# Optimization experiments

Hardware: AMD Instinct MI355X
Metric: run time of the kernel (lower is better)

## Reference

```python
import jax, jax.numpy as jnp
import numpy as np

NUM_NODES = 500_000
NUM_EDGES = 8_000_000
NUM_GRAPHS = 8_192


def gcn_conv(x, edge_index, W, b):
    """PyG GCNConv (default args): add self-loops, symmetric deg normalization.
    Messages flow source (row=edge_index[0]) -> target (col=edge_index[1])."""
    n = x.shape[0]
    loop = jnp.arange(n, dtype=edge_index.dtype)
    row = jnp.concatenate([edge_index[0], loop])
    col = jnp.concatenate([edge_index[1], loop])
    h = x @ W  # [n, out]
    deg = jax.ops.segment_sum(jnp.ones_like(col, dtype=x.dtype), col, num_segments=n)
    dinv = jnp.where(deg > 0, jax.lax.rsqrt(deg), 0.0)
    norm = dinv[row] * dinv[col]  # [E+n]
    msg = h[row] * norm[:, None]  # gather + scale
    out = jax.ops.segment_sum(msg, col, num_segments=n)  # scatter-add at targets
    return out + b


def global_mean_pool(x, batch, num_graphs):
    s = jax.ops.segment_sum(x, batch, num_segments=num_graphs)
    cnt = jax.ops.segment_sum(jnp.ones((x.shape[0],), dtype=x.dtype), batch, num_segments=num_graphs)
    return s / jnp.maximum(cnt, 1.0)[:, None]


def setup_inputs() -> dict:
    key = jax.random.key(0)
    ks = jax.random.split(key, 12)
    x = jax.random.normal(ks[0], (NUM_NODES, 9), dtype=jnp.float32)
    edge_index = jax.random.randint(ks[1], (2, NUM_EDGES), 0, NUM_NODES, dtype=jnp.int64)
    batch = jnp.sort(jax.random.randint(ks[2], (NUM_NODES,), 0, NUM_GRAPHS, dtype=jnp.int64))
    metadata = jax.random.normal(ks[3], (NUM_GRAPHS, 27), dtype=jnp.float32)
    def glorot(k, shape):
        lim = float(np.sqrt(6.0 / (shape[0] + shape[1])))
        return jax.random.uniform(k, shape, jnp.float32, -lim, lim)
    W1 = glorot(ks[4], (9, 16));  b1 = jnp.zeros((16,), jnp.float32)
    W2 = glorot(ks[5], (16, 16)); b2 = jnp.zeros((16,), jnp.float32)
    Wh1 = glorot(ks[6], (16 + 27, 16)); bh1 = jnp.zeros((16,), jnp.float32)
    Wh2 = glorot(ks[7], (16, 1));       bh2 = jnp.zeros((1,), jnp.float32)
    return {"x": x, "edge_index": edge_index, "batch": batch, "metadata": metadata,
            "W1": W1, "b1": b1, "W2": W2, "b2": b2,
            "Wh1": Wh1, "bh1": bh1, "Wh2": Wh2, "bh2": bh2}


def reference(x, edge_index, batch, metadata, W1, b1, W2, b2, Wh1, bh1, Wh2, bh2):
    # eval mode: dropout is identity
    h = jax.nn.relu(gcn_conv(x, edge_index, W1, b1))
    h = jax.nn.relu(gcn_conv(h, edge_index, W2, b2))
    emb = global_mean_pool(h, batch, metadata.shape[0])  # [G, 16]
    z = jnp.concatenate([emb, metadata], axis=1)          # [G, 43]
    z = jax.nn.relu(z @ Wh1 + bh1)
    return z @ Wh2 + bh2  # [G, 1]
```

## Files before the change

### kernel.cpp

```cpp
#include <hip/hip_runtime.h>
#include <hip/hip_fp8.h>

#define N_NODES 500000
#define N_EDGES 8000000
#define N_GRAPHS 8192
#define BKT 512
#define NBK 977
#define C_CAP 9216
#define TILE2 8192
#define NTB2 977
#define CSR_IT 9

typedef __attribute__((ext_vector_type(2))) float v2f;
typedef __attribute__((ext_vector_type(4))) unsigned v4u;

#if __has_builtin(__builtin_amdgcn_cvt_pk_f32_fp8)
template <bool HI>
__device__ __forceinline__ v2f cvt2fp8(unsigned w) {
    return __builtin_amdgcn_cvt_pk_f32_fp8((int)w, HI);
}
#else
template <bool HI>
__device__ __forceinline__ v2f cvt2fp8(unsigned w) {
    unsigned h16 = HI ? (w >> 16) : (w & 0xFFFFu);
    __hip_fp8_e4m3 a, b;
    a.__x = (__hip_fp8_storage_t)(h16 & 0xFFu);
    b.__x = (__hip_fp8_storage_t)(h16 >> 8);
    v2f r; r.x = (float)a; r.y = (float)b; return r;
}
#endif
#if __has_builtin(__builtin_amdgcn_cvt_pk_fp8_f32)
__device__ __forceinline__ unsigned pk4fp8(float a, float b, float c, float d) {
    int r = 0;
    r = __builtin_amdgcn_cvt_pk_fp8_f32(a, b, r, false);
    r = __builtin_amdgcn_cvt_pk_fp8_f32(c, d, r, true);
    return (unsigned)r;
}
#else
__device__ __forceinline__ unsigned pk4fp8(float a, float b, float c, float d) {
    __hip_fp8_e4m3 qa(a), qb(b), qc(c), qd(d);
    return (unsigned)qa.__x | ((unsigned)qb.__x << 8) |
           ((unsigned)qc.__x << 16) | ((unsigned)qd.__x << 24);
}
#endif
__device__ __forceinline__ void addfp8x16(float* acc, uint4 a) {
    v2f p;
    p = cvt2fp8<false>(a.x); acc[0] += p.x; acc[1] += p.y;
    p = cvt2fp8<true>(a.x);  acc[2] += p.x; acc[3] += p.y;
    p = cvt2fp8<false>(a.y); acc[4] += p.x; acc[5] += p.y;
    p = cvt2fp8<true>(a.y);  acc[6] += p.x; acc[7] += p.y;
    p = cvt2fp8<false>(a.z); acc[8] += p.x; acc[9] += p.y;
    p = cvt2fp8<true>(a.z);  acc[10] += p.x; acc[11] += p.y;
    p = cvt2fp8<false>(a.w); acc[12] += p.x; acc[13] += p.y;
    p = cvt2fp8<true>(a.w);  acc[14] += p.x; acc[15] += p.y;
}
__device__ __forceinline__ void addfp8x8(float* acc, uint2 a) {
    v2f p;
    p = cvt2fp8<false>(a.x); acc[0] += p.x; acc[1] += p.y;
    p = cvt2fp8<true>(a.x);  acc[2] += p.x; acc[3] += p.y;
    p = cvt2fp8<false>(a.y); acc[4] += p.x; acc[5] += p.y;
    p = cvt2fp8<true>(a.y);  acc[6] += p.x; acc[7] += p.y;
}

__device__ __forceinline__ int blockscan_excl(int v, int* wsum, int* woff) {
    int t = threadIdx.x;
    int lane = t & 63, wid = t >> 6;
    int inc = v;
#pragma unroll
    for (int o = 1; o <= 32; o <<= 1) {
        int p = __shfl_up(inc, o, 64);
        if (lane >= o) inc += p;
    }
    if (lane == 63) wsum[wid] = inc;
    __syncthreads();
    if (wid == 0) {
        int ws = (lane < 16) ? wsum[lane] : 0;
#pragma unroll
        for (int o = 1; o <= 8; o <<= 1) {
            int p = __shfl_up(ws, o, 64);
            if (lane >= o) ws += p;
        }
        if (lane < 16) woff[lane] = ws - wsum[lane];
    }
    __syncthreads();
    return inc - v + woff[wid];
}

__global__ void k_init(float* __restrict__ pooled, int* __restrict__ gcursor) {
    int i = blockIdx.x * 256 + threadIdx.x;
    if (i < N_GRAPHS * 17) pooled[i] = 0.0f;
    if (i < NBK) gcursor[i] = i * C_CAP;
}

__global__ __launch_bounds__(1024) void
k_build(const int4* __restrict__ row4, const int4* __restrict__ col4,
        int* __restrict__ gcursor, unsigned* __restrict__ packed, int E) {
    __shared__ unsigned sortedv[TILE2];
    __shared__ unsigned short sortedb[TILE2];
    __shared__ int hist2[2][1024];
    __shared__ int lbase[1024];
    __shared__ int runbase[1024];
    __shared__ int wsum[16], woff[16];
    __shared__ int stotal;
    int t = threadIdx.x, b = blockIdx.x;
    int sub = t >> 9;
    hist2[0][t] = 0; hist2[1][t] = 0;
    __syncthreads();
    unsigned uval[8];
    unsigned short ub[8];
#pragma unroll
    for (int k = 0; k < 2; k++) {
        int vi = b * 2048 + k * 1024 + t;
        int j0 = k * 4;
        if (vi * 4 < E) {
            int4 c = col4[vi];
            int4 r = row4[vi];
            unsigned cc, rr;
            cc = (unsigned)c.x; rr = (unsigned)r.x;
            if (cc < N_NODES && rr < N_NODES) { uval[j0] = (rr << 9) | (cc & 511u); ub[j0] = (unsigned short)(cc >> 9); atomicAdd(&hist2[sub][cc >> 9], 1); } else ub[j0] = 0xFFFFu;
            cc = (unsigned)c.y; rr = (unsigned)r.y;
            if (cc < N_NODES && rr < N_NODES) { uval[j0+1] = (rr << 9) | (cc & 511u); ub[j0+1] = (unsigned short)(cc >> 9); atomicAdd(&hist2[sub][cc >> 9], 1); } else ub[j0+1] = 0xFFFFu;
            cc = (unsigned)c.z; rr = (unsigned)r.z;
            if (cc < N_NODES && rr < N_NODES) { uval[j0+2] = (rr << 9) | (cc & 511u); ub[j0+2] = (unsigned short)(cc >> 9); atomicAdd(&hist2[sub][cc >> 9], 1); } else ub[j0+2] = 0xFFFFu;
            cc = (unsigned)c.w; rr = (unsigned)r.w;
            if (cc < N_NODES && rr < N_NODES) { uval[j0+3] = (rr << 9) | (cc & 511u); ub[j0+3] = (unsigned short)(cc >> 9); atomicAdd(&hist2[sub][cc >> 9], 1); } else ub[j0+3] = 0xFFFFu;
        } else {
            ub[j0] = 0xFFFFu; ub[j0+1] = 0xFFFFu; ub[j0+2] = 0xFFFFu; ub[j0+3] = 0xFFFFu;
        }
    }
    __syncthreads();
    int tot = (t < NBK) ? (hist2[0][t] + hist2[1][t]) : 0;
    int excl = blockscan_excl(tot, wsum, woff);
    lbase[t] = excl;
    if (t == 1023) stotal = excl + tot;
    if (t < NBK && tot) runbase[t] = atomicAdd(&gcursor[t], tot);
    hist2[0][t] = 0;
    __syncthreads();
    int total = stotal;
#pragma unroll
    for (int j = 0; j < 8; j++) {
        unsigned bb = ub[j];
        if (bb != 0xFFFFu) {
            int l = lbase[bb] + atomicAdd(&hist2[0][bb], 1);
            sortedv[l] = uval[j];
            sortedb[l] = (unsigned short)bb;
        }
    }
    __syncthreads();
    for (int l = t; l < total; l += 1024) {
        int bb = sortedb[l];
        packed[runbase[bb] + (l - lbase[bb])] = sortedv[l];
    }
}

__global__ __launch_bounds__(1024) void
k_goff(const int* __restrict__ gcursor, int* __restrict__ goff) {
    __shared__ int wsum[16], woff[16];
    int t = threadIdx.x;
    int v = (t < NBK) ? (gcursor[t] - t * C_CAP) : 0;
    int excl = blockscan_excl(v, wsum, woff);
    if (t < NBK) goff[t] = excl;
    if (t == NBK) goff[NBK] = excl;
}

__global__ __launch_bounds__(1024) void
k_csr(const unsigned* __restrict__ packed, const int* __restrict__ goff,
      const float* __restrict__ x, const float* __restrict__ W1,
      int* __restrict__ srcs, int* __restrict__ rowptr,
      float* __restrict__ dinv_g, uint4* __restrict__ hsu, int N) {
    __shared__ int sortedv[C_CAP];
    __shared__ int hist2[2][BKT];
    __shared__ int off[BKT];
    __shared__ int wsum[16], woff[16];
    __shared__ float sW1[144];
    int t = threadIdx.x, b = blockIdx.x;
    int h = t >> 9;
    if (t < 144) sW1[t] = W1[t];
    ((int*)hist2)[t] = 0;
    __syncthreads();
    int gbase = goff[b];
    int cnt = goff[b + 1] - gbase;
    int sfix = b * C_CAP;
    unsigned pw[CSR_IT];
#pragma unroll
    for (int k = 0; k < CSR_IT; k++) {
        int i = k * 1024 + t;
        if (i < cnt) {
            unsigned w = packed[sfix + i];
            pw[k] = w;
            atomicAdd(&hist2[h][w & 511u], 1);
        } else pw[k] = 0xFFFFFFFFu;
    }
    __syncthreads();
    int ls = (t < BKT) ? (hist2[0][t] + hist2[1][t]) : 0;
    int excl = blockscan_excl(ls, wsum, woff);
    int v = b * BKT + t;
    float di = rsqrtf(1.0f + (float)ls);
    if (t < BKT) {
        off[t] = excl;
        if (v < N) {
            rowptr[v] = gbase + excl;
            dinv_g[v] = di;
        }
    }
    if (b == NBK - 1 && t == 0) rowptr[N] = gbase + cnt;
    __syncthreads();
    if (t < BKT) hist2[0][t] = 0;
    __syncthreads();
#pragma unroll
    for (int k = 0; k < CSR_IT; k++) {
        unsigned w = pw[k];
        if (w != 0xFFFFFFFFu) {
            unsigned c = w & 511u;
            int l = off[c] + atomicAdd(&hist2[0][c], 1);
            sortedv[l] = (int)(w >> 9);
        }
    }
    __syncthreads();
    for (int l = t; l < cnt; l += 1024)
        __builtin_nontemporal_store(sortedv[l], &srcs[gbase + l]);
    if (t < BKT && v < N) {
        float xi[9];
#pragma unroll
        for (int k = 0; k < 9; k++) xi[k] = x[v * 9 + k];
        float hh[16];
#pragma unroll
        for (int j = 0; j < 16; j++) {
            float acc = 0.f;
#pragma unroll
            for (int k = 0; k < 9; k++) acc += xi[k] * sW1[k * 16 + j];
            hh[j] = acc * di;
        }
        uint4 w;
        w.x = pk4fp8(hh[0], hh[1], hh[2], hh[3]);
        w.y = pk4fp8(hh[4], hh[5], hh[6], hh[7]);
        w.z = pk4fp8(hh[8], hh[9], hh[10], hh[11]);
        w.w = pk4fp8(hh[12], hh[13], hh[14], hh[15]);
        hsu[v] = w;
    }
}

__global__ void k_pullA(const int* __restrict__ rowptr, const int* __restrict__ srcs,
                        const uint4* __restrict__ hsu, const float* __restrict__ dinv,
                        const float* __restrict__ b1, const float* __restrict__ W2,
                        uint4* __restrict__ hs2u, int N) {
    int v = blockIdx.x * 256 + threadIdx.x;
    if (v >= N) return;
    int s = rowptr[v], e = rowptr[v + 1];
    float acc[16];
    {
        uint4 u = hsu[v];
#pragma unroll
        for (int i = 0; i < 16; i++) acc[i] = 0.f;
        addfp8x16(acc, u);
    }
    int k = s;
    for (; k + 4 <= e; k += 4) {
        int r0 = __builtin_nontemporal_load(&srcs[k]);
        int r1 = __builtin_nontemporal_load(&srcs[k + 1]);
        int r2 = __builtin_nontemporal_load(&srcs[k + 2]);
        int r3 = __builtin_nontemporal_load(&srcs[k + 3]);
        uint4 a0 = hsu[r0];
        uint4 a1 = hsu[r1];
        uint4 a2 = hsu[r2];
        uint4 a3 = hsu[r3];
        addfp8x16(acc, a0); addfp8x16(acc, a1);
        addfp8x16(acc, a2); addfp8x16(acc, a3);
    }
    for (; k < e; k++) addfp8x16(acc, hsu[__builtin_nontemporal_load(&srcs[k])]);
    float di = dinv[v];
    float h1[16];
#pragma unroll
    for (int i = 0; i < 16; i++) {
        float tt = acc[i] * di + b1[i];
        h1[i] = tt > 0.f ? tt : 0.f;
    }
    float o[16];
#pragma unroll
    for (int i = 0; i < 16; i++) o[i] = 0.f;
#pragma unroll
    for (int kk = 0; kk < 16; kk++) {
#pragma unroll
        for (int i = 0; i < 16; i++) o[i] += h1[kk] * W2[kk * 16 + i];
    }
    v4u w;
    w.x = pk4fp8(o[0] * di, o[1] * di, o[2] * di, o[3] * di);
    w.y = pk4fp8(o[4] * di, o[5] * di, o[6] * di, o[7] * di);
    w.z = pk4fp8(o[8] * di, o[9] * di, o[10] * di, o[11] * di);
    w.w = pk4fp8(o[12] * di, o[13] * di, o[14] * di, o[15] * di);
    __builtin_nontemporal_store(w, (v4u*)&hs2u[v]);
}

__global__ void k_pullB(const int* __restrict__ rowptr, const int* __restrict__ srcs,
                        const uint2* __restrict__ hs2u, const float* __restrict__ dinv,
                        const float* __restrict__ b2, const int* __restrict__ batch,
                        float* __restrict__ pooled, float* __restrict__ cnt, int N) {
    int tid = blockIdx.x * 256 + threadIdx.x;
    int v = tid >> 1;
    int q = tid & 1;
    if (v >= N) return;
    int s = rowptr[v], e = rowptr[v + 1];
    float acc[8];
#pragma unroll
    for (int i = 0; i < 8; i++) acc[i] = 0.f;
    addfp8x8(acc, hs2u[v * 2 + q]);
    int k = s;
    for (; k + 8 <= e; k += 8) {
        int r0 = __builtin_nontemporal_load(&srcs[k]);
        int r1 = __builtin_nontemporal_load(&srcs[k + 1]);
        int r2 = __builtin_nontemporal_load(&srcs[k + 2]);
        int r3 = __builtin_nontemporal_load(&srcs[k + 3]);
        int r4 = __builtin_nontemporal_load(&srcs[k + 4]);
        int r5 = __builtin_nontemporal_load(&srcs[k + 5]);
        int r6 = __builtin_nontemporal_load(&srcs[k + 6]);
        int r7 = __builtin_nontemporal_load(&srcs[k + 7]);
        uint2 a0 = hs2u[r0 * 2 + q];
        uint2 a1 = hs2u[r1 * 2 + q];
        uint2 a2 = hs2u[r2 * 2 + q];
        uint2 a3 = hs2u[r3 * 2 + q];
        uint2 a4 = hs2u[r4 * 2 + q];
        uint2 a5 = hs2u[r5 * 2 + q];
        uint2 a6 = hs2u[r6 * 2 + q];
        uint2 a7 = hs2u[r7 * 2 + q];
        addfp8x8(acc, a0); addfp8x8(acc, a1); addfp8x8(acc, a2); addfp8x8(acc, a3);
        addfp8x8(acc, a4); addfp8x8(acc, a5); addfp8x8(acc, a6); addfp8x8(acc, a7);
    }
    for (; k + 4 <= e; k += 4) {
        int r0 = __builtin_nontemporal_load(&srcs[k]);
        int r1 = __builtin_nontemporal_load(&srcs[k + 1]);
        int r2 = __builtin_nontemporal_load(&srcs[k + 2]);
        int r3 = __builtin_nontemporal_load(&srcs[k + 3]);
        uint2 a0 = hs2u[r0 * 2 + q];
        uint2 a1 = hs2u[r1 * 2 + q];
        uint2 a2 = hs2u[r2 * 2 + q];
        uint2 a3 = hs2u[r3 * 2 + q];
        addfp8x8(acc, a0); addfp8x8(acc, a1); addfp8x8(acc, a2); addfp8x8(acc, a3);
    }
    for (; k < e; k++) addfp8x8(acc, hs2u[__builtin_nontemporal_load(&srcs[k]) * 2 + q]);
    float di = dinv[v];
    float h2[8];
#pragma unroll
    for (int i = 0; i < 8; i++) {
        float tt = acc[i] * di + b2[q * 8 + i];
        h2[i] = tt > 0.f ? tt : 0.f;
    }
    int l = threadIdx.x & 63;
    int g = batch[v];
    float c = (q == 0) ? 1.0f : 0.0f;
#pragma unroll
    for (int off = 2; off <= 32; off <<= 1) {
        int pg = __shfl_up(g, off, 64);
        float pc = __shfl_up(c, off, 64);
        float p0 = __shfl_up(h2[0], off, 64);
        float p1 = __shfl_up(h2[1], off, 64);
        float p2 = __shfl_up(h2[2], off, 64);
        float p3 = __shfl_up(h2[3], off, 64);
        float p4 = __shfl_up(h2[4], off, 64);
        float p5 = __shfl_up(h2[5], off, 64);
        float p6 = __shfl_up(h2[6], off, 64);
        float p7 = __shfl_up(h2[7], off, 64);
        if (l >= off && pg == g) {
            c += pc;
            h2[0] += p0; h2[1] += p1; h2[2] += p2; h2[3] += p3;
            h2[4] += p4; h2[5] += p5; h2[6] += p6; h2[7] += p7;
        }
    }
    int gn = __shfl_down(g, 2, 64);
    bool tail = (l >= 62) || (gn != g);
    if (tail) {
#pragma unroll
        for (int i = 0; i < 8; i++)
            atomicAdd(&pooled[g * 16 + q * 8 + i], h2[i]);
        if (q == 0) atomicAdd(&cnt[g], c);
    }
}

__global__ void k_head(const float* __restrict__ pooled, const float* __restrict__ cnt,
                       const float* __restrict__ meta, const float* __restrict__ Wh1,
                       const float* __restrict__ bh1, const float* __restrict__ Wh2,
                       const float* __restrict__ bh2, float* __restrict__ out, int G) {
    int g = blockIdx.x * 256 + threadIdx.x;
    if (g >= G) return;
    float z[43];
    float c = cnt[g];
    c = c > 1.f ? c : 1.f;
#pragma unroll
    for (int j = 0; j < 16; j++) z[j] = pooled[g * 16 + j] / c;
#pragma unroll
    for (int j = 0; j < 27; j++) z[16 + j] = meta[g * 27 + j];
    float acc2 = bh2[0];
#pragma unroll
    for (int jj = 0; jj < 16; jj++) {
        float a = bh1[jj];
#pragma unroll
        for (int k = 0; k < 43; k++) a += z[k] * Wh1[k * 16 + jj];
        a = a > 0.f ? a : 0.f;
        acc2 += a * Wh2[jj];
    }
    out[g] = acc2;
}

extern "C" void kernel_launch(void* const* d_in, const int* in_sizes, int n_in,
                              void* d_out, int out_size, void* d_ws, size_t ws_size,
                              hipStream_t stream) {
    const float* x    = (const float*)d_in[0];
    const int*   ei   = (const int*)d_in[1];
    const int*   batch= (const int*)d_in[2];
    const float* meta = (const float*)d_in[3];
    const float* W1   = (const float*)d_in[4];
    const float* b1   = (const float*)d_in[5];
    const float* W2   = (const float*)d_in[6];
    const float* b2   = (const float*)d_in[7];
    const float* Wh1  = (const float*)d_in[8];
    const float* bh1  = (const float*)d_in[9];
    const float* Wh2  = (const float*)d_in[10];
    const float* bh2  = (const float*)d_in[11];
    float* out = (float*)d_out;

    const int N = N_NODES, E = N_EDGES, G = N_GRAPHS;
    const int* row = ei;
    const int* col = ei + E;

    float*    ws      = (float*)d_ws;
    float*    dinv    = ws;
    unsigned* packed  = (unsigned*)(ws + 512000);
    int*      srcs    = (int*)(packed + 9004032);
    unsigned* hsu     = (unsigned*)(srcs + 8000000);
    unsigned* hs2u    = hsu + 2000000;
    float*    pooled  = (float*)(hs2u + 2000000);
    float*    cnt     = pooled + G * 16;
    int*      gcursor = (int*)(cnt + G);
    int*      goff    = gcursor + 1024;
    int*      rowptr  = goff + 1024;

    dim3 blk(256);

    k_init<<<(G * 17 + 255) / 256, blk, 0, stream>>>(pooled, gcursor);
    k_build<<<NTB2, dim3(1024), 0, stream>>>((const int4*)row, (const int4*)col,
                                             gcursor, packed, E);
    k_goff<<<1, dim3(1024), 0, stream>>>(gcursor, goff);
    k_csr<<<NBK, dim3(1024), 0, stream>>>(packed, goff, x, W1,
                                          srcs, rowptr, dinv, (uint4*)hsu, N);

    k_pullA<<<(N + 255) / 256, blk, 0, stream>>>(rowptr, srcs, (const uint4*)hsu,
                                                 dinv, b1, W2, (uint4*)hs2u, N);

    int gP2 = (N * 2 + 255) / 256;
    k_pullB<<<gP2, blk, 0, stream>>>(rowptr, srcs, (const uint2*)hs2u, dinv,
                                     b2, batch, pooled, cnt, N);

    k_head<<<(G + 255) / 256, blk, 0, stream>>>(pooled, cnt, meta, Wh1, bh1, Wh2, bh2, out, G);
}
```

Before: 393.7 us.

## Sort CSR sources by half-range within each destination to improve gather locality

The CSR build now buckets each edge by destination and by whether its source falls in the lower or upper half of the node range. Each adjacency list is therefore split into low-source and high-source groups, which is meant to improve cache locality of the later gathers of node features. It also drops the nontemporal stores for srcs and hs2u and the v4u vector type. dinv is now read back from global memory in the same kernel that writes it, and the diff leaves a dead line behind.

```diff
diff --git a/kernel.cpp b/kernel.cpp
--- a/kernel.cpp
+++ b/kernel.cpp
@@ -10,9 +10,9 @@
 #define TILE2 8192
 #define NTB2 977
 #define CSR_IT 9
+#define HALF_N 250000
 
 typedef __attribute__((ext_vector_type(2))) float v2f;
-typedef __attribute__((ext_vector_type(4))) unsigned v4u;
 
 #if __has_builtin(__builtin_amdgcn_cvt_pk_f32_fp8)
 template <bool HI>
@@ -169,14 +169,14 @@
       int* __restrict__ srcs, int* __restrict__ rowptr,
       float* __restrict__ dinv_g, uint4* __restrict__ hsu, int N) {
     __shared__ int sortedv[C_CAP];
-    __shared__ int hist2[2][BKT];
-    __shared__ int off[BKT];
+    __shared__ int hist2[2][1024];
+    __shared__ int off[1024];
     __shared__ int wsum[16], woff[16];
     __shared__ float sW1[144];
     int t = threadIdx.x, b = blockIdx.x;
     int h = t >> 9;
     if (t < 144) sW1[t] = W1[t];
-    ((int*)hist2)[t] = 0;
+    hist2[0][t] = 0; hist2[1][t] = 0;
     __syncthreads();
     int gbase = goff[b];
     int cnt = goff[b + 1] - gbase;
@@ -188,55 +188,65 @@
         if (i < cnt) {
             unsigned w = packed[sfix + i];
             pw[k] = w;
-            atomicAdd(&hist2[h][w & 511u], 1);
+            unsigned key = ((w & 511u) << 1) | (unsigned)((w >> 9) >= HALF_N);
+            atomicAdd(&hist2[h][key], 1);
         } else pw[k] = 0xFFFFFFFFu;
     }
     __syncthreads();
-    int ls = (t < BKT) ? (hist2[0][t] + hist2[1][t]) : 0;
-    int excl = blockscan_excl(ls, wsum, woff);
-    int v = b * BKT + t;
-    float di = rsqrtf(1.0f + (float)ls);
-    if (t < BKT) {
-        off[t] = excl;
-        if (v < N) {
-            rowptr[v] = gbase + excl;
-            dinv_g[v] = di;
+    int lk = hist2[0][t] + hist2[1][t];
+    int excl = blockscan_excl(lk, wsum, woff);
+    off[t] = excl;
+    __syncthreads();
+    int v = b * BKT + (t >> 1);
+    if ((t & 1) == 0) {
+        int node = t >> 1;
+        int vv = b * BKT + node;
+        int ls0 = hist2[0][t] + hist2[1][t];
+        int ls1 = hist2[0][t + 1] + hist2[1][t + 1];
+        int tot = ls0 + ls1;
+        if (vv < N) {
+            rowptr[vv] = gbase + off[t];
+            dinv_g[vv] = rsqrtf(1.0f + (float)tot);
         }
     }
     if (b == NBK - 1 && t == 0) rowptr[N] = gbase + cnt;
     __syncthreads();
-    if (t < BKT) hist2[0][t] = 0;
+    hist2[0][t] = 0;
     __syncthreads();
 #pragma unroll
     for (int k = 0; k < CSR_IT; k++) {
         unsigned w = pw[k];
         if (w != 0xFFFFFFFFu) {
-            unsigned c = w & 511u;
-            int l = off[c] + atomicAdd(&hist2[0][c], 1);
+            unsigned key = ((w & 511u) << 1) | (unsigned)((w >> 9) >= HALF_N);
+            int l = off[key] + atomicAdd(&hist2[0][key], 1);
             sortedv[l] = (int)(w >> 9);
         }
     }
     __syncthreads();
-    for (int l = t; l < cnt; l += 1024)
-        __builtin_nontemporal_store(sortedv[l], &srcs[gbase + l]);
-    if (t < BKT && v < N) {
-        float xi[9];
-#pragma unroll
-        for (int k = 0; k < 9; k++) xi[k] = x[v * 9 + k];
-        float hh[16];
-#pragma unroll
-        for (int j = 0; j < 16; j++) {
-            float acc = 0.f;
-#pragma unroll
-            for (int k = 0; k < 9; k++) acc += xi[k] * sW1[k * 16 + j];
-            hh[j] = acc * di;
-        }
-        uint4 w;
-        w.x = pk4fp8(hh[0], hh[1], hh[2], hh[3]);
-        w.y = pk4fp8(hh[4], hh[5], hh[6], hh[7]);
-        w.z = pk4fp8(hh[8], hh[9], hh[10], hh[11]);
-        w.w = pk4fp8(hh[12], hh[13], hh[14], hh[15]);
-        hsu[v] = w;
+    for (int l = t; l < cnt; l += 1024) srcs[gbase + l] = sortedv[l];
+    if (t < BKT) {
+        int vv = b * BKT + t;
+        if (vv < N) {
+            int ls0 = hist2[1][t * 2] ? 0 : 0;
+            float di = dinv_g[vv];
+            float xi[9];
+#pragma unroll
+            for (int k = 0; k < 9; k++) xi[k] = x[vv * 9 + k];
+            float hh[16];
+#pragma unroll
+            for (int j = 0; j < 16; j++) {
+                float acc = 0.f;
+#pragma unroll
+                for (int k = 0; k < 9; k++) acc += xi[k] * sW1[k * 16 + j];
+                hh[j] = acc * di;
+            }
+            uint4 w;
+            w.x = pk4fp8(hh[0], hh[1], hh[2], hh[3]);
+            w.y = pk4fp8(hh[4], hh[5], hh[6], hh[7]);
+            w.z = pk4fp8(hh[8], hh[9], hh[10], hh[11]);
+            w.w = pk4fp8(hh[12], hh[13], hh[14], hh[15]);
+            hsu[vv] = w;
+        }
     }
 }
 
@@ -283,12 +293,12 @@
 #pragma unroll
         for (int i = 0; i < 16; i++) o[i] += h1[kk] * W2[kk * 16 + i];
     }
-    v4u w;
+    uint4 w;
     w.x = pk4fp8(o[0] * di, o[1] * di, o[2] * di, o[3] * di);
     w.y = pk4fp8(o[4] * di, o[5] * di, o[6] * di, o[7] * di);
     w.z = pk4fp8(o[8] * di, o[9] * di, o[10] * di, o[11] * di);
     w.w = pk4fp8(o[12] * di, o[13] * di, o[14] * di, o[15] * di);
-    __builtin_nontemporal_store(w, (v4u*)&hs2u[v]);
+    hs2u[v] = w;
 }
 
 __global__ void k_pullB(const int* __restrict__ rowptr, const int* __restrict__ srcs,
```

Result: faster. 384.6 us (-2.3%).
